# Kernel tuning notes

Measured on AMD Instinct MI355X. Metric: run time of the kernel, lower is better.

## Reference

```python
import jax, jax.numpy as jnp
import numpy as np


def setup_inputs() -> dict:
    key = jax.random.key(0)
    kx, ky = jax.random.split(key)
    B, SX, SY, D = 8, 2048, 2048, 512
    x = jax.random.normal(kx, (B, SX, D), dtype=jnp.float32)
    y = jax.random.normal(ky, (B, SY, D), dtype=jnp.float32)
    return {"x": x, "y": y}


def reference(x, y):
    # e = x @ y^T : [B, Sx, Sy]
    e = jnp.einsum("bsd,btd->bst", x, y)
    ai = jax.nn.softmax(e, axis=-1)
    # a = ai @ y : [B, Sx, D]
    a = jnp.einsum("bst,btd->bsd", ai, y)
    # concat [x, a] along feature dim -> [B, Sx, 2D]; dropout in eval mode = identity
    out = jnp.concatenate([x, a], axis=-1)
    return out
```

## Files before the change

kernel.cpp:

```cpp
#include <hip/hip_runtime.h>
#include <stdint.h>

typedef _Float16 half4v __attribute__((ext_vector_type(4)));
typedef _Float16 half8v __attribute__((ext_vector_type(8)));
typedef float    f32x4  __attribute__((ext_vector_type(4)));
typedef __attribute__((address_space(3))) void       lds_void;
typedef const __attribute__((address_space(1))) void g_void;

#define NB 8
#define SXX 2048
#define DD 512
#define QBLK 64
#define TBLK 64
#define NITER 32

#define RSB 1072u
#define BUFSZ (64u * RSB)
#define POFF  (2u * BUFSZ)
#define PR    152u
#define SCOFF (POFF + 64u * PR)
#define TMOFF (SCOFF + 256u)
#define LOFF  (TMOFF + 1024u)
#define LDS_BYTES 149248
#define YH_BYTES (8ull * 2048ull * 512ull * 2ull)

__global__ __launch_bounds__(256)
void convert_y(const float* __restrict__ y, _Float16* __restrict__ yh) {
  const int i = (blockIdx.x * 256 + threadIdx.x) * 8;
  f32x4 f0 = *(const f32x4*)(y + i);
  f32x4 f1 = *(const f32x4*)(y + i + 4);
  half8v h;
  h[0]=(_Float16)f0[0]; h[1]=(_Float16)f0[1]; h[2]=(_Float16)f0[2]; h[3]=(_Float16)f0[3];
  h[4]=(_Float16)f1[0]; h[5]=(_Float16)f1[1]; h[6]=(_Float16)f1[2]; h[7]=(_Float16)f1[3];
  *(half8v*)(yh + i) = h;
}

template <bool USE_WS>
__global__ __launch_bounds__(512)
void attn_fused(const float* __restrict__ x, const float* __restrict__ y,
                const _Float16* __restrict__ yh, float* __restrict__ out) {
  extern __shared__ char smem[];
  const int bid   = blockIdx.x;
  const int b     = bid & 7;
  const int qtile = bid >> 3;
  const int tid   = threadIdx.x;
  const int w     = tid >> 6;
  const int lane  = tid & 63;
  const int l15   = lane & 15;
  const int g     = lane >> 4;
  const int qg    = w & 1;
  const int tq    = w >> 1;

  const float*    xb  = x + (size_t)b * SXX * DD;
  const float*    yb  = y + (size_t)b * SXX * DD;
  const _Float16* yhb = USE_WS ? (yh + (size_t)b * SXX * DD) : nullptr;
  float* outb = out + (size_t)b * SXX * (2 * DD);
  const int qbase = qtile * QBLK;

  if (USE_WS) {
#pragma unroll
    for (int i = 0; i < 8; ++i) {
      const int row = w * 8 + i;
      __builtin_amdgcn_global_load_lds((g_void*)(yhb + row * DD + lane * 8),
                                       (lds_void*)(smem + (uint32_t)row * RSB), 16, 0, 0);
    }
  }

  {
    const f32x4* src = (const f32x4*)(xb + (size_t)qbase * DD);
    for (int i = tid; i < QBLK * (DD / 4); i += 512) {
      f32x4 v = src[i];
      *(f32x4*)(outb + (size_t)(qbase + (i >> 7)) * (2 * DD) + (i & 127) * 4) = v;
    }
  }

  half8v bq0[16], bq1[16];
  {
    const float* xr0 = xb + (size_t)(qbase + qg * 32 + l15) * DD;
    const float* xr1 = xr0 + 16 * DD;
#pragma unroll
    for (int c = 0; c < 16; ++c) {
      const int d0 = c * 32 + g * 8;
      f32x4 f0 = *(const f32x4*)(xr0 + d0);
      f32x4 f1 = *(const f32x4*)(xr0 + d0 + 4);
      half8v h;
      h[0]=(_Float16)f0[0]; h[1]=(_Float16)f0[1]; h[2]=(_Float16)f0[2]; h[3]=(_Float16)f0[3];
      h[4]=(_Float16)f1[0]; h[5]=(_Float16)f1[1]; h[6]=(_Float16)f1[2]; h[7]=(_Float16)f1[3];
      bq0[c] = h;
      f0 = *(const f32x4*)(xr1 + d0);
      f1 = *(const f32x4*)(xr1 + d0 + 4);
      h[0]=(_Float16)f0[0]; h[1]=(_Float16)f0[1]; h[2]=(_Float16)f0[2]; h[3]=(_Float16)f0[3];
      h[4]=(_Float16)f1[0]; h[5]=(_Float16)f1[1]; h[6]=(_Float16)f1[2]; h[7]=(_Float16)f1[3];
      bq1[c] = h;
    }
  }

  if (!USE_WS) {
#pragma unroll
    for (int k = 0; k < 8; ++k) {
      const int u = tid + k * 512;
      const int t = u >> 6, c8 = u & 63;
      const float* p = yb + t * DD + c8 * 8;
      f32x4 f0 = *(const f32x4*)p, f1 = *(const f32x4*)(p + 4);
      half8v h;
      h[0]=(_Float16)f0[0]; h[1]=(_Float16)f0[1]; h[2]=(_Float16)f0[2]; h[3]=(_Float16)f0[3];
      h[4]=(_Float16)f1[0]; h[5]=(_Float16)f1[1]; h[6]=(_Float16)f1[2]; h[7]=(_Float16)f1[3];
      *(half8v*)(smem + (uint32_t)t * RSB + (uint32_t)c8 * 16u) = h;
    }
  }

  f32x4 acc[4][4];
#pragma unroll
  for (int i = 0; i < 4; ++i)
#pragma unroll
    for (int j = 0; j < 4; ++j) acc[i][j] = (f32x4){0.f, 0.f, 0.f, 0.f};
  float mrun0 = -3.0e38f, mrun1 = -3.0e38f, lrun0 = 0.0f, lrun1 = 0.0f;

  __syncthreads();

  for (int it = 0; it < NITER; ++it) {
    const uint32_t cb  = (uint32_t)(it & 1) * BUFSZ;
    const uint32_t nb2 = cb ^ BUFSZ;

    if (USE_WS && it + 1 < NITER) {
      const _Float16* src = yhb + (size_t)(it + 1) * TBLK * DD;
#pragma unroll
      for (int i = 0; i < 8; ++i) {
        const int row = w * 8 + i;
        __builtin_amdgcn_global_load_lds((g_void*)(src + row * DD + lane * 8),
                                         (lds_void*)(smem + nb2 + (uint32_t)row * RSB), 16, 0, 0);
      }
    }

    f32x4 st0 = (f32x4){0.f, 0.f, 0.f, 0.f};
    f32x4 st1 = (f32x4){0.f, 0.f, 0.f, 0.f};
#pragma unroll
    for (int c = 0; c < 16; ++c) {
      const half8v af = *(const half8v*)(smem + cb +
          (uint32_t)(tq * 16 + l15) * RSB + 64u * (uint32_t)c + 16u * (uint32_t)g);
      st0 = __builtin_amdgcn_mfma_f32_16x16x32_f16(af, bq0[c], st0, 0, 0, 0);
      st1 = __builtin_amdgcn_mfma_f32_16x16x32_f16(af, bq1[c], st1, 0, 0, 0);
    }

    float tmax0 = fmaxf(fmaxf(st0[0], st0[1]), fmaxf(st0[2], st0[3]));
    float tmax1 = fmaxf(fmaxf(st1[0], st1[1]), fmaxf(st1[2], st1[3]));
    tmax0 = fmaxf(tmax0, __shfl_xor(tmax0, 16));
    tmax0 = fmaxf(tmax0, __shfl_xor(tmax0, 32));
    tmax1 = fmaxf(tmax1, __shfl_xor(tmax1, 16));
    tmax1 = fmaxf(tmax1, __shfl_xor(tmax1, 32));
    if (g == 0) {
      ((float*)(smem + TMOFF))[tq * 64 + qg * 32 + l15]      = tmax0;
      ((float*)(smem + TMOFF))[tq * 64 + qg * 32 + 16 + l15] = tmax1;
    }
    __syncthreads();
    const float* tmb = (const float*)(smem + TMOFF);
    const int qi0 = qg * 32 + l15, qi1 = qi0 + 16;
    const float mnew0 = fmaxf(mrun0,
        fmaxf(fmaxf(tmb[qi0], tmb[64 + qi0]), fmaxf(tmb[128 + qi0], tmb[192 + qi0])));
    const float mnew1 = fmaxf(mrun1,
        fmaxf(fmaxf(tmb[qi1], tmb[64 + qi1]), fmaxf(tmb[128 + qi1], tmb[192 + qi1])));

    float rs0 = 0.f, rs1 = 0.f;
    half4v hv0, hv1;
#pragma unroll
    for (int r = 0; r < 4; ++r) {
      const float e0 = __expf(st0[r] - mnew0); rs0 += e0; hv0[r] = (_Float16)e0;
      const float e1 = __expf(st1[r] - mnew1); rs1 += e1; hv1[r] = (_Float16)e1;
    }
    rs0 += __shfl_xor(rs0, 16); rs0 += __shfl_xor(rs0, 32);
    rs1 += __shfl_xor(rs1, 16); rs1 += __shfl_xor(rs1, 32);
    const float scale0 = __expf(mrun0 - mnew0);
    const float scale1 = __expf(mrun1 - mnew1);
    lrun0 = lrun0 * scale0 + rs0;  mrun0 = mnew0;
    lrun1 = lrun1 * scale1 + rs1;  mrun1 = mnew1;

    *(half4v*)(smem + POFF + (uint32_t)qi0 * PR + (uint32_t)(tq * 32 + g * 8)) = hv0;
    *(half4v*)(smem + POFF + (uint32_t)qi1 * PR + (uint32_t)(tq * 32 + g * 8)) = hv1;
    if (tq == 0 && g == 0) {
      ((float*)(smem + SCOFF))[qi0] = scale0;
      ((float*)(smem + SCOFF))[qi1] = scale1;
    }

    if (!USE_WS && it + 1 < NITER) {
      const float* ybt = yb + (size_t)(it + 1) * TBLK * DD;
#pragma unroll
      for (int k = 0; k < 8; ++k) {
        const int u = tid + k * 512;
        const int t = u >> 6, c8 = u & 63;
        const float* p = ybt + t * DD + c8 * 8;
        f32x4 f0 = *(const f32x4*)p, f1 = *(const f32x4*)(p + 4);
        half8v h;
        h[0]=(_Float16)f0[0]; h[1]=(_Float16)f0[1]; h[2]=(_Float16)f0[2]; h[3]=(_Float16)f0[3];
        h[4]=(_Float16)f1[0]; h[5]=(_Float16)f1[1]; h[6]=(_Float16)f1[2]; h[7]=(_Float16)f1[3];
        *(half8v*)(smem + nb2 + (uint32_t)t * RSB + (uint32_t)c8 * 16u) = h;
      }
    }

    __syncthreads();

    {
#pragma unroll
      for (int qq = 0; qq < 4; ++qq) {
        const f32x4 s4 = *(const f32x4*)(smem + SCOFF + (uint32_t)(qq * 16 + 4 * g) * 4u);
#pragma unroll
        for (int dtl = 0; dtl < 4; ++dtl) {
          acc[qq][dtl][0] *= s4[0]; acc[qq][dtl][1] *= s4[1];
          acc[qq][dtl][2] *= s4[2]; acc[qq][dtl][3] *= s4[3];
        }
      }
      __builtin_amdgcn_sched_barrier(0);

      const uint32_t pb = POFF + (uint32_t)l15 * PR + (uint32_t)g * 8u;
      const uint32_t tb = cb + (uint32_t)(4 * g + (l15 >> 2)) * RSB +
                          (uint32_t)(l15 & 3) * 8u + (uint32_t)w * 128u;
#pragma unroll
      for (int ch = 0; ch < 2; ++ch) {
        half4v palo[4], pahi[4];
#pragma unroll
        for (int qq = 0; qq < 4; ++qq) {
          const uint32_t a = pb + (uint32_t)qq * (16u * PR) + (uint32_t)ch * 64u;
          asm volatile("ds_read_b64 %0, %1" : "=v"(palo[qq]) : "v"(a));
          asm volatile("ds_read_b64 %0, %1" : "=v"(pahi[qq]) : "v"(a + 32u));
        }
        half4v blo[4], bhi[4];
#pragma unroll
        for (int dtl = 0; dtl < 4; ++dtl) {
          const uint32_t a = tb + (uint32_t)ch * (32u * RSB) + (uint32_t)dtl * 32u;
          asm volatile("ds_read_b64_tr_b16 %0, %1" : "=v"(blo[dtl]) : "v"(a));
          asm volatile("ds_read_b64_tr_b16 %0, %1" : "=v"(bhi[dtl]) : "v"(a + 16u * RSB));
        }
        asm volatile("s_waitcnt lgkmcnt(0)" ::: "memory");
        __builtin_amdgcn_sched_barrier(0);
#pragma unroll
        for (int dtl = 0; dtl < 4; ++dtl) {
          const half8v b8 = __builtin_shufflevector(blo[dtl], bhi[dtl], 0, 1, 2, 3, 4, 5, 6, 7);
#pragma unroll
          for (int qq = 0; qq < 4; ++qq) {
            const half8v pa = __builtin_shufflevector(palo[qq], pahi[qq],
                                                      0, 1, 2, 3, 4, 5, 6, 7);
            acc[qq][dtl] = __builtin_amdgcn_mfma_f32_16x16x32_f16(pa, b8, acc[qq][dtl], 0, 0, 0);
          }
        }
      }
    }
    __syncthreads();
  }

  if (g == 0) {
    ((float*)(smem + LOFF))[tq * 64 + qg * 32 + l15]      = lrun0;
    ((float*)(smem + LOFF))[tq * 64 + qg * 32 + 16 + l15] = lrun1;
  }
  __syncthreads();
#pragma unroll
  for (int qq = 0; qq < 4; ++qq) {
    const f32x4 l0 = *(const f32x4*)(smem + LOFF + (uint32_t)(qq * 16 + 4 * g) * 4u);
    const f32x4 l1 = *(const f32x4*)(smem + LOFF + 256u + (uint32_t)(qq * 16 + 4 * g) * 4u);
    const f32x4 l2 = *(const f32x4*)(smem + LOFF + 512u + (uint32_t)(qq * 16 + 4 * g) * 4u);
    const f32x4 l3 = *(const f32x4*)(smem + LOFF + 768u + (uint32_t)(qq * 16 + 4 * g) * 4u);
    f32x4 iv;
#pragma unroll
    for (int r = 0; r < 4; ++r) iv[r] = 1.0f / (l0[r] + l1[r] + l2[r] + l3[r]);
#pragma unroll
    for (int dtl = 0; dtl < 4; ++dtl) {
#pragma unroll
      for (int r = 0; r < 4; ++r) {
        const int q = qbase + qq * 16 + 4 * g + r;
        outb[(size_t)q * (2 * DD) + DD + w * 64 + dtl * 16 + l15] = acc[qq][dtl][r] * iv[r];
      }
    }
  }
}

extern "C" void kernel_launch(void* const* d_in, const int* in_sizes, int n_in,
                              void* d_out, int out_size, void* d_ws, size_t ws_size,
                              hipStream_t stream) {
  (void)in_sizes; (void)n_in; (void)out_size;
  const float* x = (const float*)d_in[0];
  const float* y = (const float*)d_in[1];
  float* out = (float*)d_out;
  static_assert(LDS_BYTES <= 160 * 1024, "LDS over budget");
  const bool use_ws = (ws_size >= YH_BYTES);
  if (use_ws) {
    _Float16* yh = (_Float16*)d_ws;
    hipLaunchKernelGGL(convert_y, dim3(4096), dim3(256), 0, stream, y, yh);
    hipFuncSetAttribute((const void*)attn_fused<true>,
                        hipFuncAttributeMaxDynamicSharedMemorySize, LDS_BYTES);
    hipLaunchKernelGGL((attn_fused<true>), dim3((SXX / QBLK) * NB), dim3(512),
                       LDS_BYTES, stream, x, y, yh, out);
  } else {
    hipFuncSetAttribute((const void*)attn_fused<false>,
                        hipFuncAttributeMaxDynamicSharedMemorySize, LDS_BYTES);
    hipLaunchKernelGGL((attn_fused<false>), dim3((SXX / QBLK) * NB), dim3(512),
                       LDS_BYTES, stream, x, y, nullptr, out);
  }
}
```

Baseline: 140.8 us.

## Warp-specialize QK softmax and software-pipeline PV across iterations with triple buffering

```diff
diff --git a/kernel.cpp b/kernel.cpp
--- a/kernel.cpp
+++ b/kernel.cpp
@@ -11,17 +11,17 @@
 #define SXX 2048
 #define DD 512
 #define QBLK 64
-#define TBLK 64
-#define NITER 32
-
-#define RSB 1072u
-#define BUFSZ (64u * RSB)
-#define POFF  (2u * BUFSZ)
-#define PR    152u
-#define SCOFF (POFF + 64u * PR)
-#define TMOFF (SCOFF + 256u)
-#define LOFF  (TMOFF + 1024u)
-#define LDS_BYTES 149248
+#define TBLK 32
+#define NITER 64
+
+#define RSB 1040u
+#define YSZ (32u * RSB)
+#define POFF (3u * YSZ)
+#define PR 72u
+#define PSZ (64u * PR)
+#define SCOFF (POFF + 2u * PSZ)
+#define LIOFF (SCOFF + 512u)
+#define LDS_BYTES 109824
 #define YH_BYTES (8ull * 2048ull * 512ull * 2ull)
 
 __global__ __launch_bounds__(256)
@@ -37,6 +37,7 @@
 
 template <bool USE_WS>
 __global__ __launch_bounds__(512)
+__attribute__((amdgpu_waves_per_eu(2, 2)))
 void attn_fused(const float* __restrict__ x, const float* __restrict__ y,
                 const _Float16* __restrict__ yh, float* __restrict__ out) {
   extern __shared__ char smem[];
@@ -48,8 +49,6 @@
   const int lane  = tid & 63;
   const int l15   = lane & 15;
   const int g     = lane >> 4;
-  const int qg    = w & 1;
-  const int tq    = w >> 1;
 
   const float*    xb  = x + (size_t)b * SXX * DD;
   const float*    yb  = y + (size_t)b * SXX * DD;
@@ -59,8 +58,8 @@
 
   if (USE_WS) {
 #pragma unroll
-    for (int i = 0; i < 8; ++i) {
-      const int row = w * 8 + i;
+    for (int i = 0; i < 4; ++i) {
+      const int row = w * 4 + i;
       __builtin_amdgcn_global_load_lds((g_void*)(yhb + row * DD + lane * 8),
                                        (lds_void*)(smem + (uint32_t)row * RSB), 16, 0, 0);
     }
@@ -75,8 +74,8 @@
   }
 
   half8v bq0[16], bq1[16];
-  {
-    const float* xr0 = xb + (size_t)(qbase + qg * 32 + l15) * DD;
+  if (w < 2) {
+    const float* xr0 = xb + (size_t)(qbase + w * 32 + l15) * DD;
     const float* xr1 = xr0 + 16 * DD;
 #pragma unroll
     for (int c = 0; c < 16; ++c) {
@@ -95,171 +94,190 @@
     }
   }
 
-  if (!USE_WS) {
-#pragma unroll
-    for (int k = 0; k < 8; ++k) {
-      const int u = tid + k * 512;
-      const int t = u >> 6, c8 = u & 63;
-      const float* p = yb + t * DD + c8 * 8;
-      f32x4 f0 = *(const f32x4*)p, f1 = *(const f32x4*)(p + 4);
-      half8v h;
-      h[0]=(_Float16)f0[0]; h[1]=(_Float16)f0[1]; h[2]=(_Float16)f0[2]; h[3]=(_Float16)f0[3];
-      h[4]=(_Float16)f1[0]; h[5]=(_Float16)f1[1]; h[6]=(_Float16)f1[2]; h[7]=(_Float16)f1[3];
-      *(half8v*)(smem + (uint32_t)t * RSB + (uint32_t)c8 * 16u) = h;
-    }
-  }
-
-  f32x4 acc[4][4];
-#pragma unroll
-  for (int i = 0; i < 4; ++i)
-#pragma unroll
-    for (int j = 0; j < 4; ++j) acc[i][j] = (f32x4){0.f, 0.f, 0.f, 0.f};
-  float mrun0 = -3.0e38f, mrun1 = -3.0e38f, lrun0 = 0.0f, lrun1 = 0.0f;
-
-  __syncthreads();
-
-  for (int it = 0; it < NITER; ++it) {
-    const uint32_t cb  = (uint32_t)(it & 1) * BUFSZ;
-    const uint32_t nb2 = cb ^ BUFSZ;
-
-    if (USE_WS && it + 1 < NITER) {
-      const _Float16* src = yhb + (size_t)(it + 1) * TBLK * DD;
-#pragma unroll
-      for (int i = 0; i < 8; ++i) {
-        const int row = w * 8 + i;
-        __builtin_amdgcn_global_load_lds((g_void*)(src + row * DD + lane * 8),
-                                         (lds_void*)(smem + nb2 + (uint32_t)row * RSB), 16, 0, 0);
-      }
-    }
-
-    f32x4 st0 = (f32x4){0.f, 0.f, 0.f, 0.f};
-    f32x4 st1 = (f32x4){0.f, 0.f, 0.f, 0.f};
-#pragma unroll
-    for (int c = 0; c < 16; ++c) {
-      const half8v af = *(const half8v*)(smem + cb +
-          (uint32_t)(tq * 16 + l15) * RSB + 64u * (uint32_t)c + 16u * (uint32_t)g);
-      st0 = __builtin_amdgcn_mfma_f32_16x16x32_f16(af, bq0[c], st0, 0, 0, 0);
-      st1 = __builtin_amdgcn_mfma_f32_16x16x32_f16(af, bq1[c], st1, 0, 0, 0);
-    }
-
-    float tmax0 = fmaxf(fmaxf(st0[0], st0[1]), fmaxf(st0[2], st0[3]));
-    float tmax1 = fmaxf(fmaxf(st1[0], st1[1]), fmaxf(st1[2], st1[3]));
-    tmax0 = fmaxf(tmax0, __shfl_xor(tmax0, 16));
-    tmax0 = fmaxf(tmax0, __shfl_xor(tmax0, 32));
-    tmax1 = fmaxf(tmax1, __shfl_xor(tmax1, 16));
-    tmax1 = fmaxf(tmax1, __shfl_xor(tmax1, 32));
-    if (g == 0) {
-      ((float*)(smem + TMOFF))[tq * 64 + qg * 32 + l15]      = tmax0;
-      ((float*)(smem + TMOFF))[tq * 64 + qg * 32 + 16 + l15] = tmax1;
-    }
-    __syncthreads();
-    const float* tmb = (const float*)(smem + TMOFF);
-    const int qi0 = qg * 32 + l15, qi1 = qi0 + 16;
-    const float mnew0 = fmaxf(mrun0,
-        fmaxf(fmaxf(tmb[qi0], tmb[64 + qi0]), fmaxf(tmb[128 + qi0], tmb[192 + qi0])));
-    const float mnew1 = fmaxf(mrun1,
-        fmaxf(fmaxf(tmb[qi1], tmb[64 + qi1]), fmaxf(tmb[128 + qi1], tmb[192 + qi1])));
-
-    float rs0 = 0.f, rs1 = 0.f;
-    half4v hv0, hv1;
-#pragma unroll
-    for (int r = 0; r < 4; ++r) {
-      const float e0 = __expf(st0[r] - mnew0); rs0 += e0; hv0[r] = (_Float16)e0;
-      const float e1 = __expf(st1[r] - mnew1); rs1 += e1; hv1[r] = (_Float16)e1;
-    }
-    rs0 += __shfl_xor(rs0, 16); rs0 += __shfl_xor(rs0, 32);
-    rs1 += __shfl_xor(rs1, 16); rs1 += __shfl_xor(rs1, 32);
-    const float scale0 = __expf(mrun0 - mnew0);
-    const float scale1 = __expf(mrun1 - mnew1);
-    lrun0 = lrun0 * scale0 + rs0;  mrun0 = mnew0;
-    lrun1 = lrun1 * scale1 + rs1;  mrun1 = mnew1;
-
-    *(half4v*)(smem + POFF + (uint32_t)qi0 * PR + (uint32_t)(tq * 32 + g * 8)) = hv0;
-    *(half4v*)(smem + POFF + (uint32_t)qi1 * PR + (uint32_t)(tq * 32 + g * 8)) = hv1;
-    if (tq == 0 && g == 0) {
-      ((float*)(smem + SCOFF))[qi0] = scale0;
-      ((float*)(smem + SCOFF))[qi1] = scale1;
-    }
-
-    if (!USE_WS && it + 1 < NITER) {
-      const float* ybt = yb + (size_t)(it + 1) * TBLK * DD;
-#pragma unroll
-      for (int k = 0; k < 8; ++k) {
-        const int u = tid + k * 512;
-        const int t = u >> 6, c8 = u & 63;
-        const float* p = ybt + t * DD + c8 * 8;
+  if (!USE_WS && w >= 2) {
+#pragma unroll
+    for (int i = 0; i < 6; ++i) {
+      const int row = (w - 2) + 6 * i;
+      if (row < 32) {
+        const float* p = yb + row * DD + lane * 8;
         f32x4 f0 = *(const f32x4*)p, f1 = *(const f32x4*)(p + 4);
         half8v h;
         h[0]=(_Float16)f0[0]; h[1]=(_Float16)f0[1]; h[2]=(_Float16)f0[2]; h[3]=(_Float16)f0[3];
         h[4]=(_Float16)f1[0]; h[5]=(_Float16)f1[1]; h[6]=(_Float16)f1[2]; h[7]=(_Float16)f1[3];
-        *(half8v*)(smem + nb2 + (uint32_t)t * RSB + (uint32_t)c8 * 16u) = h;
-      }
-    }
+        *(half8v*)(smem + (uint32_t)row * RSB + (uint32_t)lane * 16u) = h;
+      }
+    }
+  }
+
+  f32x4 acc[4][4];
+#pragma unroll
+  for (int i = 0; i < 4; ++i)
+#pragma unroll
+    for (int j = 0; j < 4; ++j) acc[i][j] = (f32x4){0.f, 0.f, 0.f, 0.f};
+  float mrun0 = -3.0e38f, mrun1 = -3.0e38f, lrun0 = 0.0f, lrun1 = 0.0f;
+
+  __syncthreads();
+
+  auto pv_step = [&](uint32_t ybo, uint32_t pbo, uint32_t sco) {
+#pragma unroll
+    for (int qq = 0; qq < 4; ++qq) {
+      const f32x4 s4 = *(const f32x4*)(smem + sco + (uint32_t)(qq * 16 + 4 * g) * 4u);
+#pragma unroll
+      for (int dtl = 0; dtl < 4; ++dtl) {
+        acc[qq][dtl][0] *= s4[0]; acc[qq][dtl][1] *= s4[1];
+        acc[qq][dtl][2] *= s4[2]; acc[qq][dtl][3] *= s4[3];
+      }
+    }
+    __builtin_amdgcn_sched_barrier(0);
+    half4v palo[4], pahi[4];
+#pragma unroll
+    for (int qq = 0; qq < 4; ++qq) {
+      const uint32_t a = pbo + (uint32_t)(qq * 16 + l15) * PR + (uint32_t)g * 8u;
+      asm volatile("ds_read_b64 %0, %1" : "=v"(palo[qq]) : "v"(a));
+      asm volatile("ds_read_b64 %0, %1" : "=v"(pahi[qq]) : "v"(a + 32u));
+    }
+    asm volatile("s_waitcnt lgkmcnt(0)" ::: "memory");
+    __builtin_amdgcn_sched_barrier(0);
+    half8v pa8[4];
+#pragma unroll
+    for (int qq = 0; qq < 4; ++qq)
+      pa8[qq] = __builtin_shufflevector(palo[qq], pahi[qq], 0, 1, 2, 3, 4, 5, 6, 7);
+    const uint32_t tb = ybo + (uint32_t)(4 * g + (l15 >> 2)) * RSB +
+                        (uint32_t)(l15 & 3) * 8u + (uint32_t)w * 128u;
+    half4v blo[2], bhi[2];
+    asm volatile("ds_read_b64_tr_b16 %0, %1" : "=v"(blo[0]) : "v"(tb));
+    asm volatile("ds_read_b64_tr_b16 %0, %1" : "=v"(bhi[0]) : "v"(tb + 16u * RSB));
+#pragma unroll
+    for (int dtl = 0; dtl < 4; ++dtl) {
+      const int cur = dtl & 1, nxt = cur ^ 1;
+      if (dtl < 3) {
+        const uint32_t a2 = tb + (uint32_t)(dtl + 1) * 32u;
+        asm volatile("ds_read_b64_tr_b16 %0, %1" : "=v"(blo[nxt]) : "v"(a2));
+        asm volatile("ds_read_b64_tr_b16 %0, %1" : "=v"(bhi[nxt]) : "v"(a2 + 16u * RSB));
+        asm volatile("s_waitcnt lgkmcnt(2)" ::: "memory");
+      } else {
+        asm volatile("s_waitcnt lgkmcnt(0)" ::: "memory");
+      }
+      __builtin_amdgcn_sched_barrier(0);
+      const half8v b8 = __builtin_shufflevector(blo[cur], bhi[cur], 0, 1, 2, 3, 4, 5, 6, 7);
+#pragma unroll
+      for (int qq = 0; qq < 4; ++qq)
+        acc[qq][dtl] = __builtin_amdgcn_mfma_f32_16x16x32_f16(pa8[qq], b8, acc[qq][dtl], 0, 0, 0);
+    }
+  };
+
+  for (int it = 0; it < NITER; ++it) {
+    const uint32_t yb_cur  = (uint32_t)(it % 3) * YSZ;
+    const uint32_t yb_prev = (uint32_t)((it + 2) % 3) * YSZ;
+    const uint32_t yb_next = (uint32_t)((it + 1) % 3) * YSZ;
+    const uint32_t pb_cur  = POFF + (uint32_t)(it & 1) * PSZ;
+    const uint32_t pb_prev = POFF + (uint32_t)((it + 1) & 1) * PSZ;
+    const uint32_t sc_cur  = SCOFF + (uint32_t)(it & 1) * 256u;
+    const uint32_t sc_prev = SCOFF + (uint32_t)((it + 1) & 1) * 256u;
+
+    if (USE_WS && it + 1 < NITER) {
+      const _Float16* src = yhb + (size_t)(it + 1) * TBLK * DD;
+#pragma unroll
+      for (int i = 0; i < 4; ++i) {
+        const int row = w * 4 + i;
+        __builtin_amdgcn_global_load_lds((g_void*)(src + row * DD + lane * 8),
+                                         (lds_void*)(smem + yb_next + (uint32_t)row * RSB), 16, 0, 0);
+      }
+    }
+
+    if (w < 2) {
+      f32x4 st00 = (f32x4){0,0,0,0}, st01 = (f32x4){0,0,0,0};
+      f32x4 st10 = (f32x4){0,0,0,0}, st11 = (f32x4){0,0,0,0};
+#pragma unroll
+      for (int c = 0; c < 16; ++c) {
+        const uint32_t db = yb_cur + 64u * (uint32_t)c + 16u * (uint32_t)g;
+        const half8v af0 = *(const half8v*)(smem + (uint32_t)l15 * RSB + db);
+        st00 = __builtin_amdgcn_mfma_f32_16x16x32_f16(af0, bq0[c], st00, 0, 0, 0);
+        st10 = __builtin_amdgcn_mfma_f32_16x16x32_f16(af0, bq1[c], st10, 0, 0, 0);
+        const half8v af1 = *(const half8v*)(smem + (uint32_t)(16 + l15) * RSB + db);
+        st01 = __builtin_amdgcn_mfma_f32_16x16x32_f16(af1, bq0[c], st01, 0, 0, 0);
+        st11 = __builtin_amdgcn_mfma_f32_16x16x32_f16(af1, bq1[c], st11, 0, 0, 0);
+      }
+      {
+        float tm = -3.0e38f;
+#pragma unroll
+        for (int r = 0; r < 4; ++r) tm = fmaxf(tm, fmaxf(st00[r], st01[r]));
+        tm = fmaxf(tm, __shfl_xor(tm, 16));
+        tm = fmaxf(tm, __shfl_xor(tm, 32));
+        const float mnew = fmaxf(mrun0, tm);
+        float rsum = 0.f;
+        half4v h0, h1;
+#pragma unroll
+        for (int r = 0; r < 4; ++r) {
+          const float e0 = __expf(st00[r] - mnew); rsum += e0; h0[r] = (_Float16)e0;
+          const float e1 = __expf(st01[r] - mnew); rsum += e1; h1[r] = (_Float16)e1;
+        }
+        rsum += __shfl_xor(rsum, 16);
+        rsum += __shfl_xor(rsum, 32);
+        const float sc = __expf(mrun0 - mnew);
+        lrun0 = lrun0 * sc + rsum;  mrun0 = mnew;
+        const uint32_t pr = pb_cur + (uint32_t)(w * 32 + l15) * PR + (uint32_t)g * 8u;
+        *(half4v*)(smem + pr)       = h0;
+        *(half4v*)(smem + pr + 32u) = h1;
+        if (g == 0) *(float*)(smem + sc_cur + (uint32_t)(w * 32 + l15) * 4u) = sc;
+      }
+      {
+        float tm = -3.0e38f;
+#pragma unroll
+        for (int r = 0; r < 4; ++r) tm = fmaxf(tm, fmaxf(st10[r], st11[r]));
+        tm = fmaxf(tm, __shfl_xor(tm, 16));
+        tm = fmaxf(tm, __shfl_xor(tm, 32));
+        const float mnew = fmaxf(mrun1, tm);
+        float rsum = 0.f;
+        half4v h0, h1;
+#pragma unroll
+        for (int r = 0; r < 4; ++r) {
+          const float e0 = __expf(st10[r] - mnew); rsum += e0; h0[r] = (_Float16)e0;
+          const float e1 = __expf(st11[r] - mnew); rsum += e1; h1[r] = (_Float16)e1;
+        }
+        rsum += __shfl_xor(rsum, 16);
+        rsum += __shfl_xor(rsum, 32);
+        const float sc = __expf(mrun1 - mnew);
+        lrun1 = lrun1 * sc + rsum;  mrun1 = mnew;
+        const uint32_t pr = pb_cur + (uint32_t)(w * 32 + 16 + l15) * PR + (uint32_t)g * 8u;
+        *(half4v*)(smem + pr)       = h0;
+        *(half4v*)(smem + pr + 32u) = h1;
+        if (g == 0) *(float*)(smem + sc_cur + (uint32_t)(w * 32 + 16 + l15) * 4u) = sc;
+      }
+    }
+
+    if (!USE_WS && it + 1 < NITER && w >= 2) {
+      const float* ybt = yb + (size_t)(it + 1) * TBLK * DD;
+#pragma unroll
+      for (int i = 0; i < 6; ++i) {
+        const int row = (w - 2) + 6 * i;
+        if (row < 32) {
+          const float* p = ybt + row * DD + lane * 8;
+          f32x4 f0 = *(const f32x4*)p, f1 = *(const f32x4*)(p + 4);
+          half8v h;
+          h[0]=(_Float16)f0[0]; h[1]=(_Float16)f0[1]; h[2]=(_Float16)f0[2]; h[3]=(_Float16)f0[3];
+          h[4]=(_Float16)f1[0]; h[5]=(_Float16)f1[1]; h[6]=(_Float16)f1[2]; h[7]=(_Float16)f1[3];
+          *(half8v*)(smem + yb_next + (uint32_t)row * RSB + (uint32_t)lane * 16u) = h;
+        }
+      }
+    }
+
+    if (it > 0) pv_step(yb_prev, pb_prev, sc_prev);
 
     __syncthreads();
-
-    {
-#pragma unroll
-      for (int qq = 0; qq < 4; ++qq) {
-        const f32x4 s4 = *(const f32x4*)(smem + SCOFF + (uint32_t)(qq * 16 + 4 * g) * 4u);
-#pragma unroll
-        for (int dtl = 0; dtl < 4; ++dtl) {
-          acc[qq][dtl][0] *= s4[0]; acc[qq][dtl][1] *= s4[1];
-          acc[qq][dtl][2] *= s4[2]; acc[qq][dtl][3] *= s4[3];
-        }
-      }
-      __builtin_amdgcn_sched_barrier(0);
-
-      const uint32_t pb = POFF + (uint32_t)l15 * PR + (uint32_t)g * 8u;
-      const uint32_t tb = cb + (uint32_t)(4 * g + (l15 >> 2)) * RSB +
-                          (uint32_t)(l15 & 3) * 8u + (uint32_t)w * 128u;
-#pragma unroll
-      for (int ch = 0; ch < 2; ++ch) {
-        half4v palo[4], pahi[4];
-#pragma unroll
-        for (int qq = 0; qq < 4; ++qq) {
-          const uint32_t a = pb + (uint32_t)qq * (16u * PR) + (uint32_t)ch * 64u;
-          asm volatile("ds_read_b64 %0, %1" : "=v"(palo[qq]) : "v"(a));
-          asm volatile("ds_read_b64 %0, %1" : "=v"(pahi[qq]) : "v"(a + 32u));
-        }
-        half4v blo[4], bhi[4];
-#pragma unroll
-        for (int dtl = 0; dtl < 4; ++dtl) {
-          const uint32_t a = tb + (uint32_t)ch * (32u * RSB) + (uint32_t)dtl * 32u;
-          asm volatile("ds_read_b64_tr_b16 %0, %1" : "=v"(blo[dtl]) : "v"(a));
-          asm volatile("ds_read_b64_tr_b16 %0, %1" : "=v"(bhi[dtl]) : "v"(a + 16u * RSB));
-        }
-        asm volatile("s_waitcnt lgkmcnt(0)" ::: "memory");
-        __builtin_amdgcn_sched_barrier(0);
-#pragma unroll
-        for (int dtl = 0; dtl < 4; ++dtl) {
-          const half8v b8 = __builtin_shufflevector(blo[dtl], bhi[dtl], 0, 1, 2, 3, 4, 5, 6, 7);
-#pragma unroll
-          for (int qq = 0; qq < 4; ++qq) {
-            const half8v pa = __builtin_shufflevector(palo[qq], pahi[qq],
-                                                      0, 1, 2, 3, 4, 5, 6, 7);
-            acc[qq][dtl] = __builtin_amdgcn_mfma_f32_16x16x32_f16(pa, b8, acc[qq][dtl], 0, 0, 0);
-          }
-        }
-      }
-    }
-    __syncthreads();
-  }
-
-  if (g == 0) {
-    ((float*)(smem + LOFF))[tq * 64 + qg * 32 + l15]      = lrun0;
-    ((float*)(smem + LOFF))[tq * 64 + qg * 32 + 16 + l15] = lrun1;
+  }
+
+  pv_step(0u, POFF + PSZ, SCOFF + 256u);
+
+  if (w < 2 && g == 0) {
+    *(float*)(smem + LIOFF + (uint32_t)(w * 32 + l15) * 4u)        = 1.0f / lrun0;
+    *(float*)(smem + LIOFF + (uint32_t)(w * 32 + 16 + l15) * 4u)   = 1.0f / lrun1;
   }
   __syncthreads();
+
 #pragma unroll
   for (int qq = 0; qq < 4; ++qq) {
-    const f32x4 l0 = *(const f32x4*)(smem + LOFF + (uint32_t)(qq * 16 + 4 * g) * 4u);
-    const f32x4 l1 = *(const f32x4*)(smem + LOFF + 256u + (uint32_t)(qq * 16 + 4 * g) * 4u);
-    const f32x4 l2 = *(const f32x4*)(smem + LOFF + 512u + (uint32_t)(qq * 16 + 4 * g) * 4u);
-    const f32x4 l3 = *(const f32x4*)(smem + LOFF + 768u + (uint32_t)(qq * 16 + 4 * g) * 4u);
-    f32x4 iv;
-#pragma unroll
-    for (int r = 0; r < 4; ++r) iv[r] = 1.0f / (l0[r] + l1[r] + l2[r] + l3[r]);
+    const f32x4 iv = *(const f32x4*)(smem + LIOFF + (uint32_t)(qq * 16 + 4 * g) * 4u);
 #pragma unroll
     for (int dtl = 0; dtl < 4; ++dtl) {
 #pragma unroll
```

After: 259.8 us. 84.6% more time.
